# Kernel tuning notes

Measured on AMD Instinct MI355X. Metric: run time of the kernel, lower is better.

The kernel has to match this reference:

```python
import jax, jax.numpy as jnp
import numpy as np

B, N, C = 8, 8192, 64
P, K = 2048, 16
C_IN = 2 * C + 6   # 134: concat(diff, center) of (feat ++ xyz)
H1, H2 = 64, 128
EPS = 1e-5


def setup_inputs() -> dict:
    key = jax.random.key(0)
    ks = jax.random.split(key, 16)
    inp = {
        "xyz": jax.random.normal(ks[0], (B, N, 3), dtype=jnp.float32),
        "feat": jax.random.normal(ks[1], (B, C, N), dtype=jnp.float32),
        # SharedMLP layer 1: 1x1 conv + BN(eval) + ReLU
        "W1": jax.random.normal(ks[2], (H1, C_IN), dtype=jnp.float32) * (1.0 / np.sqrt(C_IN)),
        "b1": jnp.zeros((H1,), dtype=jnp.float32),
        "g1": jax.random.uniform(ks[3], (H1,), minval=0.5, maxval=1.5, dtype=jnp.float32),
        "be1": jax.random.normal(ks[4], (H1,), dtype=jnp.float32) * 0.1,
        "m1": jax.random.normal(ks[5], (H1,), dtype=jnp.float32) * 0.1,
        "v1": jax.random.uniform(ks[6], (H1,), minval=0.5, maxval=1.5, dtype=jnp.float32),
        # SharedMLP layer 2
        "W2": jax.random.normal(ks[7], (H2, H1), dtype=jnp.float32) * (1.0 / np.sqrt(H1)),
        "b2": jnp.zeros((H2,), dtype=jnp.float32),
        "g2": jax.random.uniform(ks[8], (H2,), minval=0.5, maxval=1.5, dtype=jnp.float32),
        "be2": jax.random.normal(ks[9], (H2,), dtype=jnp.float32) * 0.1,
        "m2": jax.random.normal(ks[10], (H2,), dtype=jnp.float32) * 0.1,
        "v2": jax.random.uniform(ks[11], (H2,), minval=0.5, maxval=1.5, dtype=jnp.float32),
        "npoints": P,
    }
    return inp


def _mlp_layer(x, W, b, g, be, m, v):
    # x: [b,p,k,cin] -> 1x1 conv (einsum) + eval-mode BN + ReLU
    y = jnp.einsum("bpkc,oc->bpko", x, W) + b
    y = g * (y - m) * jax.lax.rsqrt(v + EPS) + be
    return jax.nn.relu(y)


def reference(xyz, feat, W1, b1, g1, be1, m1, v1, W2, b2, g2, be2, m2, v2, npoints):
    p = npoints
    # Range sampling: take first p points
    new_xyz = xyz[:, :p]                       # [b,p,3]
    feat_t = jnp.swapaxes(feat, 1, 2)          # [b,n,c]
    feat_x = jnp.concatenate([feat_t, xyz], axis=-1)   # [b,n,c+3] (use_xyz)
    new_feat_x = feat_x[:, :p]                 # [b,p,c+3]
    # KNN via squared euclidean distance, expanded form to avoid [b,p,n,3]
    sq_q = jnp.sum(new_xyz * new_xyz, axis=-1)           # [b,p]
    sq_r = jnp.sum(xyz * xyz, axis=-1)                   # [b,n]
    dots = jnp.einsum("bpd,bnd->bpn", new_xyz, xyz)      # [b,p,n]
    d2 = sq_q[:, :, None] + sq_r[:, None, :] - 2.0 * dots
    _, idx = jax.lax.top_k(-d2, K)             # [b,p,k] nearest (ascending dist)
    # Gather neighbor features: [b,p,k,c+3]
    knn_feat = jax.vmap(lambda f, i: f[i])(feat_x, idx)
    tiled = jnp.broadcast_to(new_feat_x[:, :, None, :], knn_feat.shape)
    edge = jnp.concatenate([knn_feat - tiled, tiled], axis=-1)  # [b,p,k,2c+6]
    h = _mlp_layer(edge, W1, b1, g1, be1, m1, v1)
    h = _mlp_layer(h, W2, b2, g2, be2, m2, v2)              # [b,p,k,H2]
    new_feat = jnp.swapaxes(jnp.max(h, axis=2), 1, 2)       # [b,H2,p]
    sample_idx = jnp.broadcast_to(jnp.arange(p, dtype=jnp.int32), (xyz.shape[0], p))
    return new_xyz, new_feat, sample_idx
```

## Files before the change

kernel.cpp:

```cpp
#include <hip/hip_runtime.h>
#include <hip/hip_bf16.h>

#define BB 8
#define NN 8192
#define CC 64
#define PP 2048
#define KK 16
#define H1 64
#define H2 128
#define K2PAD 72

typedef float  f32x4 __attribute__((ext_vector_type(4)));
typedef short  s16x8 __attribute__((ext_vector_type(8)));

#define OFF_FXT   0u
#define OFF_PTS4  17825792u
#define OFF_KNN   19922944u
#define OFF_W1P   20971520u
#define OFF_W2P   20996096u
#define OFF_C1    21014528u
#define OFF_C2    21014784u

#define FLTMAX 3.402823466e+38f

static __device__ __forceinline__ unsigned short bf16b(float v) {
    __hip_bfloat16 h = __float2bfloat16(v);
    return *reinterpret_cast<unsigned short*>(&h);
}
static __device__ __forceinline__ unsigned pk2(float a, float b) {
    return ((unsigned)bf16b(b) << 16) | (unsigned)bf16b(a);
}
static __device__ __forceinline__ s16x8 as8(uint4 v) {
    union { uint4 u; s16x8 s; } x; x.u = v; return x.s;
}
#define LDS_FENCE() asm volatile("s_waitcnt lgkmcnt(0)" ::: "memory")

__global__ __launch_bounds__(512) void k1_prep(const float* __restrict__ xyz,
                                               const float* __restrict__ feat,
                                               unsigned* __restrict__ fxtb,
                                               float4* __restrict__ pts4,
                                               float* __restrict__ out0,
                                               float* __restrict__ out2) {
    __shared__ float tile[72][65];
    int b  = blockIdx.x >> 7;
    int n0 = (blockIdx.x & 127) * 64;
    int tx = threadIdx.x & 63, ty = threadIdx.x >> 6;
    for (int c = ty; c < 72; c += 8) {
        float v;
        if (c < 64)       v = feat[((size_t)b * 64 + c) * NN + n0 + tx];
        else if (c < 67)  v = xyz[((size_t)b * NN + n0 + tx) * 3 + (c - 64)];
        else              v = 0.f;
        tile[c][tx] = v;
    }
    __syncthreads();
    size_t base = ((size_t)b * NN + n0) * 36;
    for (int e = threadIdx.x; e < 64 * 36; e += 512) {
        int nl = e / 36, c = e - nl * 36;
        fxtb[base + e] = pk2(tile[2 * c][nl], tile[2 * c + 1][nl]);
    }
    if (threadIdx.x < 64) {
        int n = n0 + threadIdx.x;
        float x = tile[64][threadIdx.x], y = tile[65][threadIdx.x], z = tile[66][threadIdx.x];
        pts4[(size_t)b * NN + n] = make_float4(x, y, z, x * x + y * y + z * z);
        if (n0 < PP) out2[b * PP + n] = (float)n;
    }
    if (n0 < PP) {
        for (int e = threadIdx.x; e < 64 * 3; e += 512) {
            int nl = e / 3, d = e - nl * 3;
            out0[((size_t)b * PP + n0 + nl) * 3 + d] = tile[64 + d][nl];
        }
    }
}

__global__ __launch_bounds__(1024, 2) void k2_knn(const float4* __restrict__ pts4,
                                                  int* __restrict__ knn,
                                                  const float* __restrict__ W1, const float* __restrict__ b1,
                                                  const float* __restrict__ g1, const float* __restrict__ be1,
                                                  const float* __restrict__ m1, const float* __restrict__ v1,
                                                  const float* __restrict__ W2, const float* __restrict__ b2,
                                                  const float* __restrict__ g2, const float* __restrict__ be2,
                                                  const float* __restrict__ m2, const float* __restrict__ v2,
                                                  unsigned short* __restrict__ w1p,
                                                  unsigned short* __restrict__ w2p,
                                                  float* __restrict__ c1, float* __restrict__ c2) {
    __shared__ float4 stage[8192];
    __shared__ float2 scratch[16][2][64];
    int lane = threadIdx.x & 63;
    int wv   = threadIdx.x >> 6;
    int b    = blockIdx.x >> 5;
    int q0   = (blockIdx.x & 31) * 64 + wv * 4;
    size_t pb = (size_t)b * NN;

    float4 qc = make_float4(0.f, 0.f, 0.f, 0.f);
    if (lane < 4) qc = pts4[pb + q0 + lane];
    float qx2 = -2.f * qc.x, qy2 = -2.f * qc.y, qz2 = -2.f * qc.z;
    float bx[4], by[4], bz[4];
#pragma unroll
    for (int q = 0; q < 4; ++q) {
        bx[q] = __shfl(qx2, q); by[q] = __shfl(qy2, q); bz[q] = __shfl(qz2, q);
    }

#pragma unroll
    for (int i = 0; i < 8; ++i) {
        int p = i * 1024 + threadIdx.x;
        float4 v = pts4[pb + p];
        int r = p >> 6, c = p & 63;
        stage[(r << 6) | ((c + (r >> 1)) & 63)] = v;
    }

    if (threadIdx.x < 85) {
        int i = blockIdx.x * 85 + threadIdx.x;
        if (i < 6144) {
            int n = i / 96, c = i - n * 96;
            float s = g1[n] * rsqrtf(v1[n] + 1e-5f);
            w1p[n * 192 + c] = bf16b((c < 67) ? W1[n * 134 + c] * s : 0.f);
        } else if (i < 12288) {
            int j = i - 6144;
            int n = j / 96, c = j - n * 96;
            float s = g1[n] * rsqrtf(v1[n] + 1e-5f);
            w1p[n * 192 + 96 + c] =
                bf16b((c < 67) ? (W1[n * 134 + 67 + c] - W1[n * 134 + c]) * s : 0.f);
        } else if (i < 21504) {
            int j = i - 12288;
            int o = j / 72, k = j - o * 72;
            float s = g2[o] * rsqrtf(v2[o] + 1e-5f);
            w2p[j] = bf16b((k < 64) ? W2[o * 64 + k] * s : 0.f);
        } else if (i < 21568) {
            int l = i - 21504;
            float s = g1[l] * rsqrtf(v1[l] + 1e-5f);
            c1[l] = s * (b1[l] - m1[l]) + be1[l];
        } else if (i < 21696) {
            int p = i - 21568;
            float s = g2[p] * rsqrtf(v2[p] + 1e-5f);
            c2[p] = s * (b2[p] - m2[p]) + be2[p];
        }
    }
    __syncthreads();

    float m[4];
#pragma unroll
    for (int q = 0; q < 4; ++q) m[q] = FLTMAX;
#pragma unroll
    for (int rr = 0; rr < 2; ++rr) {
        int rowbase = (2 * lane + rr) << 6;
#pragma unroll
        for (int j8 = 0; j8 < 8; ++j8) {
            float4 cc[8];
#pragma unroll
            for (int i = 0; i < 8; ++i)
                cc[i] = stage[rowbase | ((j8 * 8 + i + lane) & 63)];
#pragma unroll
            for (int q = 0; q < 4; ++q) {
                float x = bx[q], y = by[q], z = bz[q];
#pragma unroll
                for (int i = 0; i < 8; i += 2) {
                    float e0 = fmaf(z, cc[i].z, fmaf(y, cc[i].y, fmaf(x, cc[i].x, cc[i].w)));
                    float e1 = fmaf(z, cc[i+1].z, fmaf(y, cc[i+1].y, fmaf(x, cc[i+1].x, cc[i+1].w)));
                    m[q] = fminf(fminf(m[q], e0), e1);
                }
            }
        }
    }

    float sv0 = m[0], sv1 = m[1], sv2 = m[2], sv3 = m[3];
#pragma unroll
    for (int k = 2; k <= 64; k <<= 1) {
#pragma unroll
        for (int j = k >> 1; j > 0; j >>= 1) {
            bool keepMin = (((lane & k) == 0) == ((lane & j) == 0));
            float p0 = __shfl_xor(sv0, j, 64);
            float p1 = __shfl_xor(sv1, j, 64);
            float p2 = __shfl_xor(sv2, j, 64);
            float p3 = __shfl_xor(sv3, j, 64);
            sv0 = keepMin ? fminf(sv0, p0) : fmaxf(sv0, p0);
            sv1 = keepMin ? fminf(sv1, p1) : fmaxf(sv1, p1);
            sv2 = keepMin ? fminf(sv2, p2) : fmaxf(sv2, p2);
            sv3 = keepMin ? fminf(sv3, p3) : fmaxf(sv3, p3);
        }
    }
    float T[4];
    T[0] = __shfl(sv0, 15, 64); T[1] = __shfl(sv1, 15, 64);
    T[2] = __shfl(sv2, 15, 64); T[3] = __shfl(sv3, 15, 64);

    unsigned long long below = (lane == 63) ? 0x7FFFFFFFFFFFFFFFull
                                            : ((1ull << lane) - 1ull);
#pragma unroll
    for (int pr = 0; pr < 4; pr += 2) {
        int Ms[2];
#pragma unroll
        for (int u = 0; u < 2; ++u) {
            int q = pr + u;
            float x = bx[q], y = by[q], z = bz[q], tq = T[q];
            unsigned long long rm = __ballot(m[q] <= tq);
            int cnt = 0;
            while (rm) {
                int sl = __ffsll((long long)rm) - 1; rm &= rm - 1;
                int phys = (lane + sl) & 63;
                float4 c0 = stage[((2 * sl) << 6) | phys];
                float4 c1v_ = stage[((2 * sl + 1) << 6) | phys];
                float e0 = fmaf(z, c0.z, fmaf(y, c0.y, fmaf(x, c0.x, c0.w)));
                float e1 = fmaf(z, c1v_.z, fmaf(y, c1v_.y, fmaf(x, c1v_.x, c1v_.w)));
                unsigned long long b0 = __ballot(e0 <= tq);
                if (e0 <= tq) {
                    int pos = cnt + __popcll(b0 & below);
                    if (pos < 64)
                        scratch[wv][u][pos] = make_float2(e0, __int_as_float(sl * 128 + lane));
                }
                cnt += __popcll(b0);
                unsigned long long b1 = __ballot(e1 <= tq);
                if (e1 <= tq) {
                    int pos = cnt + __popcll(b1 & below);
                    if (pos < 64)
                        scratch[wv][u][pos] = make_float2(e1, __int_as_float(sl * 128 + 64 + lane));
                }
                cnt += __popcll(b1);
            }
            Ms[u] = min(cnt, 64);
        }
        LDS_FENCE();
#pragma unroll
        for (int u = 0; u < 2; ++u) {
            int M = Ms[u];
            float2 own = scratch[wv][u][lane];
            float di = own.x; int ni = __float_as_int(own.y);
            int rank = 0;
            const float2* buf = &scratch[wv][u][0];
#pragma unroll 4
            for (int j = 0; j < M; ++j) {
                float2 e = buf[j];
                int nj = __float_as_int(e.y);
                rank += (e.x < di || (e.x == di && nj < ni)) ? 1 : 0;
            }
            if (lane < M && rank < 16)
                knn[((size_t)(b * PP + q0 + pr + u)) * KK + rank] = ni;
        }
        LDS_FENCE();
    }
}

__global__ __launch_bounds__(256, 2) void k3_mlp(const unsigned* __restrict__ fxtb,
                                                 const int* __restrict__ knn,
                                                 const unsigned short* __restrict__ w1p,
                                                 const unsigned short* __restrict__ w2p,
                                                 const float* __restrict__ c1,
                                                 const float* __restrict__ c2,
                                                 float* __restrict__ out1) {
    __shared__ __align__(16) unsigned short h1l[4][16 * K2PAD];
    __shared__ float otile[16][132];
    int lane = threadIdx.x & 63;
    int wv   = threadIdx.x >> 6;
    int b    = blockIdx.x & 7;
    int qg   = blockIdx.x >> 3;
    int qbase = qg * 16;
    int col = lane & 15, quad = lane >> 4;
    const uint4* fx4 = (const uint4*)fxtb;
    size_t rowb = (size_t)b * NN;

    f32x4 accq[4];
#pragma unroll
    for (int nt = 0; nt < 4; ++nt) accq[nt] = (f32x4){0.f, 0.f, 0.f, 0.f};
    {
        const uint4* rp = fx4 + (rowb + qbase + wv * 4 + col) * 9;
        uint4 qf0 = rp[quad];
        uint4 qf1 = rp[4 + quad];
        uint4 qf2 = rp[8];
        if (quad != 0) qf2 = make_uint4(0u, 0u, 0u, 0u);
        uint4 qf[3] = {qf0, qf1, qf2};
#pragma unroll
        for (int ks = 0; ks < 3; ++ks) {
            s16x8 a = as8(qf[ks]);
#pragma unroll
            for (int nt = 0; nt < 4; ++nt) {
                s16x8 bfr = *(const s16x8*)(w1p + (nt * 16 + col) * 192 + 96 + ks * 32 + quad * 8);
                accq[nt] = __builtin_amdgcn_mfma_f32_16x16x32_bf16(a, bfr, accq[nt], 0, 0, 0);
            }
        }
    }
    float qc[4][4];
    {
        float c1v[4];
#pragma unroll
        for (int nt = 0; nt < 4; ++nt) c1v[nt] = c1[nt * 16 + col];
#pragma unroll
        for (int qi = 0; qi < 4; ++qi)
#pragma unroll
            for (int nt = 0; nt < 4; ++nt)
                qc[qi][nt] = __shfl(accq[nt][qi], col, 64) + c1v[nt];
    }

    s16x8 w1f[3][4], w2f[2][8];
#pragma unroll
    for (int ks = 0; ks < 3; ++ks)
#pragma unroll
        for (int nt = 0; nt < 4; ++nt)
            w1f[ks][nt] = *(const s16x8*)(w1p + (nt * 16 + col) * 192 + ks * 32 + quad * 8);
#pragma unroll
    for (int ks = 0; ks < 2; ++ks)
#pragma unroll
        for (int nt = 0; nt < 8; ++nt)
            w2f[ks][nt] = *(const s16x8*)(w2p + (nt * 16 + col) * K2PAD + ks * 32 + quad * 8);
    float c2v[8];
#pragma unroll
    for (int nt = 0; nt < 8; ++nt) c2v[nt] = c2[nt * 16 + col];

    int idxAll = knn[((size_t)(b * PP + qbase + wv * 4)) * KK + lane];
    unsigned short* h1w = &h1l[wv][0];

    uint4 af[2][3];
#define PREF(buf, qi_) {                                                      \
        int nidx_ = __shfl(idxAll, (qi_) * 16 + col, 64);                     \
        const uint4* rp_ = fx4 + (rowb + nidx_) * 9;                          \
        af[buf][0] = rp_[quad];                                               \
        af[buf][1] = rp_[4 + quad];                                           \
        uint4 f2_ = rp_[8];                                                   \
        af[buf][2] = (quad == 0) ? f2_ : make_uint4(0u, 0u, 0u, 0u); }

    PREF(0, 0);

#pragma unroll
    for (int qi = 0; qi < 4; ++qi) {
        const int cur = qi & 1;
        f32x4 acc1[4];
#pragma unroll
        for (int nt = 0; nt < 4; ++nt)
            acc1[nt] = (f32x4){qc[qi][nt], qc[qi][nt], qc[qi][nt], qc[qi][nt]};
#pragma unroll
        for (int ks = 0; ks < 3; ++ks) {
            s16x8 a = as8(af[cur][ks]);
#pragma unroll
            for (int nt = 0; nt < 4; ++nt)
                acc1[nt] = __builtin_amdgcn_mfma_f32_16x16x32_bf16(a, w1f[ks][nt], acc1[nt], 0, 0, 0);
        }
        if (qi < 3) PREF(cur ^ 1, qi + 1);
#pragma unroll
        for (int nt = 0; nt < 4; ++nt)
#pragma unroll
            for (int rr = 0; rr < 4; ++rr)
                h1w[(quad * 4 + rr) * K2PAD + nt * 16 + col] = bf16b(fmaxf(acc1[nt][rr], 0.f));
        LDS_FENCE();
        f32x4 acc2[8];
#pragma unroll
        for (int nt = 0; nt < 8; ++nt) acc2[nt] = (f32x4){0.f, 0.f, 0.f, 0.f};
#pragma unroll
        for (int ks = 0; ks < 2; ++ks) {
            s16x8 a2 = *(const s16x8*)(h1w + col * K2PAD + ks * 32 + quad * 8);
#pragma unroll
            for (int nt = 0; nt < 8; ++nt)
                acc2[nt] = __builtin_amdgcn_mfma_f32_16x16x32_bf16(a2, w2f[ks][nt], acc2[nt], 0, 0, 0);
        }
#pragma unroll
        for (int nt = 0; nt < 8; ++nt) {
            float m0 = fmaxf(fmaxf(acc2[nt][0], acc2[nt][1]), fmaxf(acc2[nt][2], acc2[nt][3]));
            m0 = fmaxf(m0 + c2v[nt], 0.f);
            m0 = fmaxf(m0, __shfl_xor(m0, 16, 64));
            m0 = fmaxf(m0, __shfl_xor(m0, 32, 64));
            if (quad == 0)
                otile[wv * 4 + qi][nt * 16 + col] = m0;
        }
        LDS_FENCE();
    }
    __syncthreads();
    for (int i = threadIdx.x; i < H2 * 16; i += 256) {
        int ch = i >> 4, q = i & 15;
        out1[((size_t)(b * H2 + ch)) * PP + qbase + q] = otile[q][ch];
    }
#undef PREF
}

extern "C" void kernel_launch(void* const* d_in, const int* in_sizes, int n_in,
                              void* d_out, int out_size, void* d_ws, size_t ws_size,
                              hipStream_t stream) {
    const float* xyz  = (const float*)d_in[0];
    const float* feat = (const float*)d_in[1];
    const float* W1   = (const float*)d_in[2];
    const float* b1   = (const float*)d_in[3];
    const float* g1   = (const float*)d_in[4];
    const float* be1  = (const float*)d_in[5];
    const float* m1   = (const float*)d_in[6];
    const float* v1   = (const float*)d_in[7];
    const float* W2   = (const float*)d_in[8];
    const float* b2   = (const float*)d_in[9];
    const float* g2   = (const float*)d_in[10];
    const float* be2  = (const float*)d_in[11];
    const float* m2   = (const float*)d_in[12];
    const float* v2   = (const float*)d_in[13];

    char* ws = (char*)d_ws;
    unsigned*       fxtb = (unsigned*)(ws + OFF_FXT);
    float4*         pts4 = (float4*)(ws + OFF_PTS4);
    int*            knn  = (int*)(ws + OFF_KNN);
    unsigned short* w1p  = (unsigned short*)(ws + OFF_W1P);
    unsigned short* w2p  = (unsigned short*)(ws + OFF_W2P);
    float*          c1   = (float*)(ws + OFF_C1);
    float*          c2   = (float*)(ws + OFF_C2);

    float* out0 = (float*)d_out;
    float* out1 = out0 + (size_t)BB * PP * 3;
    float* out2 = out1 + (size_t)BB * H2 * PP;

    hipLaunchKernelGGL(k1_prep, dim3(1024), dim3(512), 0, stream,
                       xyz, feat, fxtb, pts4, out0, out2);
    hipLaunchKernelGGL(k2_knn, dim3(256), dim3(1024), 0, stream, pts4, knn,
                       W1, b1, g1, be1, m1, v1, W2, b2, g2, be2, m2, v2,
                       w1p, w2p, c1, c2);
    hipLaunchKernelGGL(k3_mlp, dim3(1024), dim3(256), 0, stream,
                       fxtb, knn, w1p, w2p, c1, c2, out1);
}
```

Baseline: 161.6 us.

## Fuse KNN and MLP kernels, keep neighbor indices and weights in LDS

Merges the KNN kernel and the MLP kernel into one 1024-thread kernel. Neighbor indices now stay in shared memory instead of making a round trip through global memory. The staging buffer is reused for padded copies of the folded weights, which are read from LDS per MFMA instead of being held in registers. Weight folding moves into the prep kernel. This cuts one launch and the global knn traffic, but the MLP phase now runs only 256 blocks of 1024 threads, and the kernel uses heavy LDS with extra LDS reads for the weights.

```diff
diff --git a/kernel.cpp b/kernel.cpp
--- a/kernel.cpp
+++ b/kernel.cpp
@@ -40,75 +40,18 @@
                                                unsigned* __restrict__ fxtb,
                                                float4* __restrict__ pts4,
                                                float* __restrict__ out0,
-                                               float* __restrict__ out2) {
+                                               float* __restrict__ out2,
+                                               const float* __restrict__ W1, const float* __restrict__ b1,
+                                               const float* __restrict__ g1, const float* __restrict__ be1,
+                                               const float* __restrict__ m1, const float* __restrict__ v1,
+                                               const float* __restrict__ W2, const float* __restrict__ b2,
+                                               const float* __restrict__ g2, const float* __restrict__ be2,
+                                               const float* __restrict__ m2, const float* __restrict__ v2,
+                                               unsigned short* __restrict__ w1p,
+                                               unsigned short* __restrict__ w2p,
+                                               float* __restrict__ c1, float* __restrict__ c2) {
     __shared__ float tile[72][65];
-    int b  = blockIdx.x >> 7;
-    int n0 = (blockIdx.x & 127) * 64;
-    int tx = threadIdx.x & 63, ty = threadIdx.x >> 6;
-    for (int c = ty; c < 72; c += 8) {
-        float v;
-        if (c < 64)       v = feat[((size_t)b * 64 + c) * NN + n0 + tx];
-        else if (c < 67)  v = xyz[((size_t)b * NN + n0 + tx) * 3 + (c - 64)];
-        else              v = 0.f;
-        tile[c][tx] = v;
-    }
-    __syncthreads();
-    size_t base = ((size_t)b * NN + n0) * 36;
-    for (int e = threadIdx.x; e < 64 * 36; e += 512) {
-        int nl = e / 36, c = e - nl * 36;
-        fxtb[base + e] = pk2(tile[2 * c][nl], tile[2 * c + 1][nl]);
-    }
-    if (threadIdx.x < 64) {
-        int n = n0 + threadIdx.x;
-        float x = tile[64][threadIdx.x], y = tile[65][threadIdx.x], z = tile[66][threadIdx.x];
-        pts4[(size_t)b * NN + n] = make_float4(x, y, z, x * x + y * y + z * z);
-        if (n0 < PP) out2[b * PP + n] = (float)n;
-    }
-    if (n0 < PP) {
-        for (int e = threadIdx.x; e < 64 * 3; e += 512) {
-            int nl = e / 3, d = e - nl * 3;
-            out0[((size_t)b * PP + n0 + nl) * 3 + d] = tile[64 + d][nl];
-        }
-    }
-}
-
-__global__ __launch_bounds__(1024, 2) void k2_knn(const float4* __restrict__ pts4,
-                                                  int* __restrict__ knn,
-                                                  const float* __restrict__ W1, const float* __restrict__ b1,
-                                                  const float* __restrict__ g1, const float* __restrict__ be1,
-                                                  const float* __restrict__ m1, const float* __restrict__ v1,
-                                                  const float* __restrict__ W2, const float* __restrict__ b2,
-                                                  const float* __restrict__ g2, const float* __restrict__ be2,
-                                                  const float* __restrict__ m2, const float* __restrict__ v2,
-                                                  unsigned short* __restrict__ w1p,
-                                                  unsigned short* __restrict__ w2p,
-                                                  float* __restrict__ c1, float* __restrict__ c2) {
-    __shared__ float4 stage[8192];
-    __shared__ float2 scratch[16][2][64];
-    int lane = threadIdx.x & 63;
-    int wv   = threadIdx.x >> 6;
-    int b    = blockIdx.x >> 5;
-    int q0   = (blockIdx.x & 31) * 64 + wv * 4;
-    size_t pb = (size_t)b * NN;
-
-    float4 qc = make_float4(0.f, 0.f, 0.f, 0.f);
-    if (lane < 4) qc = pts4[pb + q0 + lane];
-    float qx2 = -2.f * qc.x, qy2 = -2.f * qc.y, qz2 = -2.f * qc.z;
-    float bx[4], by[4], bz[4];
-#pragma unroll
-    for (int q = 0; q < 4; ++q) {
-        bx[q] = __shfl(qx2, q); by[q] = __shfl(qy2, q); bz[q] = __shfl(qz2, q);
-    }
-
-#pragma unroll
-    for (int i = 0; i < 8; ++i) {
-        int p = i * 1024 + threadIdx.x;
-        float4 v = pts4[pb + p];
-        int r = p >> 6, c = p & 63;
-        stage[(r << 6) | ((c + (r >> 1)) & 63)] = v;
-    }
-
-    if (threadIdx.x < 85) {
+    if (blockIdx.x < 256 && threadIdx.x < 85) {
         int i = blockIdx.x * 85 + threadIdx.x;
         if (i < 6144) {
             int n = i / 96, c = i - n * 96;
@@ -135,132 +78,207 @@
             c2[p] = s * (b2[p] - m2[p]) + be2[p];
         }
     }
+    int b  = blockIdx.x >> 7;
+    int n0 = (blockIdx.x & 127) * 64;
+    int tx = threadIdx.x & 63, ty = threadIdx.x >> 6;
+    for (int c = ty; c < 72; c += 8) {
+        float v;
+        if (c < 64)       v = feat[((size_t)b * 64 + c) * NN + n0 + tx];
+        else if (c < 67)  v = xyz[((size_t)b * NN + n0 + tx) * 3 + (c - 64)];
+        else              v = 0.f;
+        tile[c][tx] = v;
+    }
     __syncthreads();
-
-    float m[4];
-#pragma unroll
-    for (int q = 0; q < 4; ++q) m[q] = FLTMAX;
-#pragma unroll
-    for (int rr = 0; rr < 2; ++rr) {
-        int rowbase = (2 * lane + rr) << 6;
-#pragma unroll
-        for (int j8 = 0; j8 < 8; ++j8) {
-            float4 cc[8];
-#pragma unroll
-            for (int i = 0; i < 8; ++i)
-                cc[i] = stage[rowbase | ((j8 * 8 + i + lane) & 63)];
-#pragma unroll
-            for (int q = 0; q < 4; ++q) {
-                float x = bx[q], y = by[q], z = bz[q];
-#pragma unroll
-                for (int i = 0; i < 8; i += 2) {
-                    float e0 = fmaf(z, cc[i].z, fmaf(y, cc[i].y, fmaf(x, cc[i].x, cc[i].w)));
-                    float e1 = fmaf(z, cc[i+1].z, fmaf(y, cc[i+1].y, fmaf(x, cc[i+1].x, cc[i+1].w)));
-                    m[q] = fminf(fminf(m[q], e0), e1);
-                }
-            }
-        }
-    }
-
-    float sv0 = m[0], sv1 = m[1], sv2 = m[2], sv3 = m[3];
-#pragma unroll
-    for (int k = 2; k <= 64; k <<= 1) {
-#pragma unroll
-        for (int j = k >> 1; j > 0; j >>= 1) {
-            bool keepMin = (((lane & k) == 0) == ((lane & j) == 0));
-            float p0 = __shfl_xor(sv0, j, 64);
-            float p1 = __shfl_xor(sv1, j, 64);
-            float p2 = __shfl_xor(sv2, j, 64);
-            float p3 = __shfl_xor(sv3, j, 64);
-            sv0 = keepMin ? fminf(sv0, p0) : fmaxf(sv0, p0);
-            sv1 = keepMin ? fminf(sv1, p1) : fmaxf(sv1, p1);
-            sv2 = keepMin ? fminf(sv2, p2) : fmaxf(sv2, p2);
-            sv3 = keepMin ? fminf(sv3, p3) : fmaxf(sv3, p3);
-        }
-    }
-    float T[4];
-    T[0] = __shfl(sv0, 15, 64); T[1] = __shfl(sv1, 15, 64);
-    T[2] = __shfl(sv2, 15, 64); T[3] = __shfl(sv3, 15, 64);
-
-    unsigned long long below = (lane == 63) ? 0x7FFFFFFFFFFFFFFFull
-                                            : ((1ull << lane) - 1ull);
-#pragma unroll
-    for (int pr = 0; pr < 4; pr += 2) {
-        int Ms[2];
-#pragma unroll
-        for (int u = 0; u < 2; ++u) {
-            int q = pr + u;
-            float x = bx[q], y = by[q], z = bz[q], tq = T[q];
-            unsigned long long rm = __ballot(m[q] <= tq);
-            int cnt = 0;
-            while (rm) {
-                int sl = __ffsll((long long)rm) - 1; rm &= rm - 1;
-                int phys = (lane + sl) & 63;
-                float4 c0 = stage[((2 * sl) << 6) | phys];
-                float4 c1v_ = stage[((2 * sl + 1) << 6) | phys];
-                float e0 = fmaf(z, c0.z, fmaf(y, c0.y, fmaf(x, c0.x, c0.w)));
-                float e1 = fmaf(z, c1v_.z, fmaf(y, c1v_.y, fmaf(x, c1v_.x, c1v_.w)));
-                unsigned long long b0 = __ballot(e0 <= tq);
-                if (e0 <= tq) {
-                    int pos = cnt + __popcll(b0 & below);
-                    if (pos < 64)
-                        scratch[wv][u][pos] = make_float2(e0, __int_as_float(sl * 128 + lane));
-                }
-                cnt += __popcll(b0);
-                unsigned long long b1 = __ballot(e1 <= tq);
-                if (e1 <= tq) {
-                    int pos = cnt + __popcll(b1 & below);
-                    if (pos < 64)
-                        scratch[wv][u][pos] = make_float2(e1, __int_as_float(sl * 128 + 64 + lane));
-                }
-                cnt += __popcll(b1);
-            }
-            Ms[u] = min(cnt, 64);
-        }
-        LDS_FENCE();
-#pragma unroll
-        for (int u = 0; u < 2; ++u) {
-            int M = Ms[u];
-            float2 own = scratch[wv][u][lane];
-            float di = own.x; int ni = __float_as_int(own.y);
-            int rank = 0;
-            const float2* buf = &scratch[wv][u][0];
-#pragma unroll 4
-            for (int j = 0; j < M; ++j) {
-                float2 e = buf[j];
-                int nj = __float_as_int(e.y);
-                rank += (e.x < di || (e.x == di && nj < ni)) ? 1 : 0;
-            }
-            if (lane < M && rank < 16)
-                knn[((size_t)(b * PP + q0 + pr + u)) * KK + rank] = ni;
-        }
-        LDS_FENCE();
-    }
-}
-
-__global__ __launch_bounds__(256, 2) void k3_mlp(const unsigned* __restrict__ fxtb,
-                                                 const int* __restrict__ knn,
-                                                 const unsigned short* __restrict__ w1p,
-                                                 const unsigned short* __restrict__ w2p,
-                                                 const float* __restrict__ c1,
-                                                 const float* __restrict__ c2,
-                                                 float* __restrict__ out1) {
-    __shared__ __align__(16) unsigned short h1l[4][16 * K2PAD];
-    __shared__ float otile[16][132];
+    size_t base = ((size_t)b * NN + n0) * 36;
+    for (int e = threadIdx.x; e < 64 * 36; e += 512) {
+        int nl = e / 36, c = e - nl * 36;
+        fxtb[base + e] = pk2(tile[2 * c][nl], tile[2 * c + 1][nl]);
+    }
+    if (threadIdx.x < 64) {
+        int n = n0 + threadIdx.x;
+        float x = tile[64][threadIdx.x], y = tile[65][threadIdx.x], z = tile[66][threadIdx.x];
+        pts4[(size_t)b * NN + n] = make_float4(x, y, z, x * x + y * y + z * z);
+        if (n0 < PP) out2[b * PP + n] = (float)n;
+    }
+    if (n0 < PP) {
+        for (int e = threadIdx.x; e < 64 * 3; e += 512) {
+            int nl = e / 3, d = e - nl * 3;
+            out0[((size_t)b * PP + n0 + nl) * 3 + d] = tile[64 + d][nl];
+        }
+    }
+}
+
+__global__ __launch_bounds__(1024, 4) void k23(const float4* __restrict__ pts4,
+                                               const unsigned* __restrict__ fxtb,
+                                               const unsigned short* __restrict__ w1p,
+                                               const unsigned short* __restrict__ w2p,
+                                               const float* __restrict__ c1,
+                                               const float* __restrict__ c2,
+                                               float* __restrict__ out1) {
+    __shared__ __align__(16) char smem[131072];
+    __shared__ float2 scratch[16][2][64];
+    __shared__ int knnl[16][64];
     int lane = threadIdx.x & 63;
     int wv   = threadIdx.x >> 6;
     int b    = blockIdx.x & 7;
-    int qg   = blockIdx.x >> 3;
-    int qbase = qg * 16;
+    int q0base = (blockIdx.x >> 3) * 64;
+    size_t pb = (size_t)b * NN;
+
+    {
+        float4* stage = (float4*)smem;
+        int q0 = q0base + wv * 4;
+
+        float4 qc = make_float4(0.f, 0.f, 0.f, 0.f);
+        if (lane < 4) qc = pts4[pb + q0 + lane];
+        float qx2 = -2.f * qc.x, qy2 = -2.f * qc.y, qz2 = -2.f * qc.z;
+        float bx[4], by[4], bz[4];
+#pragma unroll
+        for (int q = 0; q < 4; ++q) {
+            bx[q] = __shfl(qx2, q); by[q] = __shfl(qy2, q); bz[q] = __shfl(qz2, q);
+        }
+
+#pragma unroll
+        for (int i = 0; i < 8; ++i) {
+            int p = i * 1024 + threadIdx.x;
+            float4 v = pts4[pb + p];
+            int r = p >> 6, c = p & 63;
+            stage[(r << 6) | ((c + (r >> 1)) & 63)] = v;
+        }
+        __syncthreads();
+
+        float m[4];
+#pragma unroll
+        for (int q = 0; q < 4; ++q) m[q] = FLTMAX;
+#pragma unroll
+        for (int rr = 0; rr < 2; ++rr) {
+            int rowbase = (2 * lane + rr) << 6;
+#pragma unroll
+            for (int j8 = 0; j8 < 8; ++j8) {
+                float4 cc[8];
+#pragma unroll
+                for (int i = 0; i < 8; ++i)
+                    cc[i] = stage[rowbase | ((j8 * 8 + i + lane) & 63)];
+#pragma unroll
+                for (int q = 0; q < 4; ++q) {
+                    float x = bx[q], y = by[q], z = bz[q];
+#pragma unroll
+                    for (int i = 0; i < 8; i += 2) {
+                        float e0 = fmaf(z, cc[i].z, fmaf(y, cc[i].y, fmaf(x, cc[i].x, cc[i].w)));
+                        float e1 = fmaf(z, cc[i+1].z, fmaf(y, cc[i+1].y, fmaf(x, cc[i+1].x, cc[i+1].w)));
+                        m[q] = fminf(fminf(m[q], e0), e1);
+                    }
+                }
+            }
+        }
+
+        float sv0 = m[0], sv1 = m[1], sv2 = m[2], sv3 = m[3];
+#pragma unroll
+        for (int k = 2; k <= 64; k <<= 1) {
+#pragma unroll
+            for (int j = k >> 1; j > 0; j >>= 1) {
+                bool keepMin = (((lane & k) == 0) == ((lane & j) == 0));
+                float p0 = __shfl_xor(sv0, j, 64);
+                float p1 = __shfl_xor(sv1, j, 64);
+                float p2 = __shfl_xor(sv2, j, 64);
+                float p3 = __shfl_xor(sv3, j, 64);
+                sv0 = keepMin ? fminf(sv0, p0) : fmaxf(sv0, p0);
+                sv1 = keepMin ? fminf(sv1, p1) : fmaxf(sv1, p1);
+                sv2 = keepMin ? fminf(sv2, p2) : fmaxf(sv2, p2);
+                sv3 = keepMin ? fminf(sv3, p3) : fmaxf(sv3, p3);
+            }
+        }
+        float T[4];
+        T[0] = __shfl(sv0, 15, 64); T[1] = __shfl(sv1, 15, 64);
+        T[2] = __shfl(sv2, 15, 64); T[3] = __shfl(sv3, 15, 64);
+
+        unsigned long long below = (lane == 63) ? 0x7FFFFFFFFFFFFFFFull
+                                                : ((1ull << lane) - 1ull);
+#pragma unroll
+        for (int pr = 0; pr < 4; pr += 2) {
+            int Ms[2];
+#pragma unroll
+            for (int u = 0; u < 2; ++u) {
+                int q = pr + u;
+                float x = bx[q], y = by[q], z = bz[q], tq = T[q];
+                unsigned long long rm = __ballot(m[q] <= tq);
+                int cnt = 0;
+                while (rm) {
+                    int sl = __ffsll((long long)rm) - 1; rm &= rm - 1;
+                    int phys = (lane + sl) & 63;
+                    float4 c0 = stage[((2 * sl) << 6) | phys];
+                    float4 c1v_ = stage[((2 * sl + 1) << 6) | phys];
+                    float e0 = fmaf(z, c0.z, fmaf(y, c0.y, fmaf(x, c0.x, c0.w)));
+                    float e1 = fmaf(z, c1v_.z, fmaf(y, c1v_.y, fmaf(x, c1v_.x, c1v_.w)));
+                    unsigned long long b0 = __ballot(e0 <= tq);
+                    if (e0 <= tq) {
+                        int pos = cnt + __popcll(b0 & below);
+                        if (pos < 64)
+                            scratch[wv][u][pos] = make_float2(e0, __int_as_float(sl * 128 + lane));
+                    }
+                    cnt += __popcll(b0);
+                    unsigned long long b1 = __ballot(e1 <= tq);
+                    if (e1 <= tq) {
+                        int pos = cnt + __popcll(b1 & below);
+                        if (pos < 64)
+                            scratch[wv][u][pos] = make_float2(e1, __int_as_float(sl * 128 + 64 + lane));
+                    }
+                    cnt += __popcll(b1);
+                }
+                Ms[u] = min(cnt, 64);
+            }
+            LDS_FENCE();
+#pragma unroll
+            for (int u = 0; u < 2; ++u) {
+                int M = Ms[u];
+                float2 own = scratch[wv][u][lane];
+                float di = own.x; int ni = __float_as_int(own.y);
+                int rank = 0;
+                const float2* buf = &scratch[wv][u][0];
+#pragma unroll 4
+                for (int j = 0; j < M; ++j) {
+                    float2 e = buf[j];
+                    int nj = __float_as_int(e.y);
+                    rank += (e.x < di || (e.x == di && nj < ni)) ? 1 : 0;
+                }
+                if (lane < M && rank < 16)
+                    knnl[wv][(pr + u) * 16 + rank] = ni;
+            }
+            LDS_FENCE();
+        }
+    }
+
+    int idxAll = knnl[wv][lane];
+
+    __syncthreads();
+
+    unsigned short* w1a   = (unsigned short*)smem;
+    unsigned short* w2l   = (unsigned short*)(smem + 13312);
+    unsigned short* h1all = (unsigned short*)(smem + 35840);
+    float*          otile = (float*)(smem + 72704);
     int col = lane & 15, quad = lane >> 4;
     const uint4* fx4 = (const uint4*)fxtb;
     size_t rowb = (size_t)b * NN;
 
+    {
+        const unsigned* src1 = (const unsigned*)w1p;
+        unsigned* d1 = (unsigned*)w1a;
+        for (int t = threadIdx.x; t < 64 * 48; t += 1024) {
+            int r = t / 48, c = t - r * 48;
+            d1[r * 52 + c] = src1[r * 96 + c];
+        }
+        const unsigned* src2 = (const unsigned*)w2p;
+        unsigned* d2 = (unsigned*)w2l;
+        for (int t = threadIdx.x; t < 128 * 36; t += 1024) {
+            int r = t / 36, c = t - r * 36;
+            d2[r * 44 + c] = src2[r * 36 + c];
+        }
+    }
+
     f32x4 accq[4];
 #pragma unroll
     for (int nt = 0; nt < 4; ++nt) accq[nt] = (f32x4){0.f, 0.f, 0.f, 0.f};
     {
-        const uint4* rp = fx4 + (rowb + qbase + wv * 4 + col) * 9;
+        const uint4* rp = fx4 + (rowb + q0base + wv * 4 + col) * 9;
         uint4 qf0 = rp[quad];
         uint4 qf1 = rp[4 + quad];
         uint4 qf2 = rp[8];
@@ -276,7 +294,7 @@
             }
         }
     }
-    float qc[4][4];
+    float qcc[4][4];
     {
         float c1v[4];
 #pragma unroll
@@ -285,26 +303,15 @@
         for (int qi = 0; qi < 4; ++qi)
 #pragma unroll
             for (int nt = 0; nt < 4; ++nt)
-                qc[qi][nt] = __shfl(accq[nt][qi], col, 64) + c1v[nt];
-    }
-
-    s16x8 w1f[3][4], w2f[2][8];
-#pragma unroll
-    for (int ks = 0; ks < 3; ++ks)
-#pragma unroll
-        for (int nt = 0; nt < 4; ++nt)
-            w1f[ks][nt] = *(const s16x8*)(w1p + (nt * 16 + col) * 192 + ks * 32 + quad * 8);
-#pragma unroll
-    for (int ks = 0; ks < 2; ++ks)
-#pragma unroll
-        for (int nt = 0; nt < 8; ++nt)
-            w2f[ks][nt] = *(const s16x8*)(w2p + (nt * 16 + col) * K2PAD + ks * 32 + quad * 8);
+                qcc[qi][nt] = __shfl(accq[nt][qi], col, 64) + c1v[nt];
+    }
     float c2v[8];
 #pragma unroll
     for (int nt = 0; nt < 8; ++nt) c2v[nt] = c2[nt * 16 + col];
 
-    int idxAll = knn[((size_t)(b * PP + qbase + wv * 4)) * KK + lane];
-    unsigned short* h1w = &h1l[wv][0];
+    __syncthreads();
+
+    unsigned short* h1w = h1all + wv * (16 * K2PAD);
 
     uint4 af[2][3];
 #define PREF(buf, qi_) {                                                      \
@@ -323,13 +330,15 @@
         f32x4 acc1[4];
 #pragma unroll
         for (int nt = 0; nt < 4; ++nt)
-            acc1[nt] = (f32x4){qc[qi][nt], qc[qi][nt], qc[qi][nt], qc[qi][nt]};
+            acc1[nt] = (f32x4){qcc[qi][nt], qcc[qi][nt], qcc[qi][nt], qcc[qi][nt]};
 #pragma unroll
         for (int ks = 0; ks < 3; ++ks) {
             s16x8 a = as8(af[cur][ks]);
 #pragma unroll
-            for (int nt = 0; nt < 4; ++nt)
-                acc1[nt] = __builtin_amdgcn_mfma_f32_16x16x32_bf16(a, w1f[ks][nt], acc1[nt], 0, 0, 0);
+            for (int nt = 0; nt < 4; ++nt) {
+                s16x8 bfr = *(const s16x8*)(w1a + (nt * 16 + col) * 104 + ks * 32 + quad * 8);
+                acc1[nt] = __builtin_amdgcn_mfma_f32_16x16x32_bf16(a, bfr, acc1[nt], 0, 0, 0);
+            }
         }
         if (qi < 3) PREF(cur ^ 1, qi + 1);
 #pragma unroll
@@ -338,31 +347,36 @@
             for (int rr = 0; rr < 4; ++rr)
                 h1w[(quad * 4 + rr) * K2PAD + nt * 16 + col] = bf16b(fmaxf(acc1[nt][rr], 0.f));
         LDS_FENCE();
-        f32x4 acc2[8];
-#pragma unroll
-        for (int nt = 0; nt < 8; ++nt) acc2[nt] = (f32x4){0.f, 0.f, 0.f, 0.f};
-#pragma unroll
-        for (int ks = 0; ks < 2; ++ks) {
-            s16x8 a2 = *(const s16x8*)(h1w + col * K2PAD + ks * 32 + quad * 8);
-#pragma unroll
-            for (int nt = 0; nt < 8; ++nt)
-                acc2[nt] = __builtin_amdgcn_mfma_f32_16x16x32_bf16(a2, w2f[ks][nt], acc2[nt], 0, 0, 0);
-        }
-#pragma unroll
-        for (int nt = 0; nt < 8; ++nt) {
-            float m0 = fmaxf(fmaxf(acc2[nt][0], acc2[nt][1]), fmaxf(acc2[nt][2], acc2[nt][3]));
-            m0 = fmaxf(m0 + c2v[nt], 0.f);
-            m0 = fmaxf(m0, __shfl_xor(m0, 16, 64));
-            m0 = fmaxf(m0, __shfl_xor(m0, 32, 64));
-            if (quad == 0)
-                otile[wv * 4 + qi][nt * 16 + col] = m0;
+#pragma unroll
+        for (int hf = 0; hf < 2; ++hf) {
+            f32x4 acc2[4];
+#pragma unroll
+            for (int nt = 0; nt < 4; ++nt) acc2[nt] = (f32x4){0.f, 0.f, 0.f, 0.f};
+#pragma unroll
+            for (int ks = 0; ks < 2; ++ks) {
+                s16x8 a2 = *(const s16x8*)(h1w + col * K2PAD + ks * 32 + quad * 8);
+#pragma unroll
+                for (int nt = 0; nt < 4; ++nt) {
+                    s16x8 wf = *(const s16x8*)(w2l + ((hf * 4 + nt) * 16 + col) * 88 + ks * 32 + quad * 8);
+                    acc2[nt] = __builtin_amdgcn_mfma_f32_16x16x32_bf16(a2, wf, acc2[nt], 0, 0, 0);
+                }
+            }
+#pragma unroll
+            for (int nt = 0; nt < 4; ++nt) {
+                float m0 = fmaxf(fmaxf(acc2[nt][0], acc2[nt][1]), fmaxf(acc2[nt][2], acc2[nt][3]));
+                m0 = fmaxf(m0 + c2v[hf * 4 + nt], 0.f);
+                m0 = fmaxf(m0, __shfl_xor(m0, 16, 64));
+                m0 = fmaxf(m0, __shfl_xor(m0, 32, 64));
+                if (quad == 0)
+                    otile[(wv * 4 + qi) * 130 + (hf * 4 + nt) * 16 + col] = m0;
+            }
         }
         LDS_FENCE();
     }
     __syncthreads();
-    for (int i = threadIdx.x; i < H2 * 16; i += 256) {
-        int ch = i >> 4, q = i & 15;
-        out1[((size_t)(b * H2 + ch)) * PP + qbase + q] = otile[q][ch];
+    for (int i = threadIdx.x; i < H2 * 64; i += 1024) {
+        int ch = i >> 6, q = i & 63;
+        out1[((size_t)(b * H2 + ch)) * PP + q0base + q] = otile[q * 130 + ch];
     }
 #undef PREF
 }
@@ -388,7 +402,6 @@
     char* ws = (char*)d_ws;
     unsigned*       fxtb = (unsigned*)(ws + OFF_FXT);
     float4*         pts4 = (float4*)(ws + OFF_PTS4);
-    int*            knn  = (int*)(ws + OFF_KNN);
     unsigned short* w1p  = (unsigned short*)(ws + OFF_W1P);
     unsigned short* w2p  = (unsigned short*)(ws + OFF_W2P);
     float*          c1   = (float*)(ws + OFF_C1);
@@ -399,10 +412,9 @@
     float* out2 = out1 + (size_t)BB * H2 * PP;
 
     hipLaunchKernelGGL(k1_prep, dim3(1024), dim3(512), 0, stream,
-                       xyz, feat, fxtb, pts4, out0, out2);
-    hipLaunchKernelGGL(k2_knn, dim3(256), dim3(1024), 0, stream, pts4, knn,
+                       xyz, feat, fxtb, pts4, out0, out2,
                        W1, b1, g1, be1, m1, v1, W2, b2, g2, be2, m2, v2,
                        w1p, w2p, c1, c2);
-    hipLaunchKernelGGL(k3_mlp, dim3(1024), dim3(256), 0, stream,
-                       fxtb, knn, w1p, w2p, c1, c2, out1);
-}
+    hipLaunchKernelGGL(k23, dim3(256), dim3(1024), 0, stream,
+                       pts4, fxtb, w1p, w2p, c1, c2, out1);
+}
```

Measured after the change: 155.3 us. 1.04x faster.
